# Performance work log

Measured on AMD Instinct MI355X. Metric: run time of the kernel, lower is better.

Reference implementation:

```python
import jax, jax.numpy as jnp
import numpy as np

N_NODES = 100000
N_EDGES = 3200000
N_GRAPHS = 2048
IN_FEATS = 64
HIDDEN = 128
EXTRA = 8


def setup_inputs() -> dict:
    key = jax.random.key(0)
    ks = jax.random.split(key, 16)
    inp = {
        "feats_node": jax.random.normal(ks[0], (N_NODES, IN_FEATS), jnp.float32),
        "feats_graph": jax.random.normal(ks[1], (N_GRAPHS, EXTRA), jnp.float32),
        "src": jax.random.randint(ks[2], (N_EDGES,), 0, N_NODES, jnp.int32),
        "dst": jax.random.randint(ks[3], (N_EDGES,), 0, N_NODES, jnp.int32),
        "graph_ids": jnp.sort(jax.random.randint(ks[4], (N_NODES,), 0, N_GRAPHS, jnp.int32)),
        # GCN weights (std=0.5 init, zero bias as in the torch module)
        "W1": jax.random.normal(ks[5], (IN_FEATS, HIDDEN), jnp.float32) * 0.5,
        "b1": jnp.zeros((HIDDEN,), jnp.float32),
        "W2": jax.random.normal(ks[6], (HIDDEN, HIDDEN), jnp.float32) * 0.5,
        "b2": jnp.zeros((HIDDEN,), jnp.float32),
        "W3": jax.random.normal(ks[7], (HIDDEN, HIDDEN), jnp.float32) * 0.5,
        "b3": jnp.zeros((HIDDEN,), jnp.float32),
        # MLP: (HIDDEN+EXTRA) -> 2*HIDDEN -> HIDDEN -> 1
        "M1": jax.random.normal(ks[8], (HIDDEN + EXTRA, 2 * HIDDEN), jnp.float32) * 0.5,
        "c1": jnp.zeros((2 * HIDDEN,), jnp.float32),
        "M2": jax.random.normal(ks[9], (2 * HIDDEN, HIDDEN), jnp.float32) * 0.5,
        "c2": jnp.zeros((HIDDEN,), jnp.float32),
        "M3": jax.random.normal(ks[10], (HIDDEN, 1), jnp.float32) * 0.5,
        "c3": jnp.zeros((1,), jnp.float32),
    }
    return inp


def _gcn_layer(h, W, b, src, dst, norm_src, norm_dst):
    # DGL GraphConv, norm='both': h' = D_in^{-1/2} A (D_out^{-1/2} h W) + b
    h = (h * norm_src[:, None]) @ W            # [N, out]
    agg = jax.ops.segment_sum(h[src], dst, num_segments=N_NODES)  # scatter-add over edges
    return agg * norm_dst[:, None] + b


def reference(feats_node, feats_graph, src, dst, graph_ids,
              W1, b1, W2, b2, W3, b3, M1, c1, M2, c2, M3, c3):
    ones_e = jnp.ones((N_EDGES,), jnp.float32)
    out_deg = jax.ops.segment_sum(ones_e, src, num_segments=N_NODES)
    in_deg = jax.ops.segment_sum(ones_e, dst, num_segments=N_NODES)
    norm_src = jax.lax.rsqrt(jnp.maximum(out_deg, 1.0))
    norm_dst = jax.lax.rsqrt(jnp.maximum(in_deg, 1.0))

    h = _gcn_layer(feats_node, W1, b1, src, dst, norm_src, norm_dst)
    h = jax.nn.selu(h)
    h = _gcn_layer(h, W2, b2, src, dst, norm_src, norm_dst)
    h = jax.nn.selu(h)
    h = _gcn_layer(h, W3, b3, src, dst, norm_src, norm_dst)
    h = jax.nn.selu(h)

    # AvgPooling readout: mean node features per graph
    sums = jax.ops.segment_sum(h, graph_ids, num_segments=N_GRAPHS)  # [G, H]
    cnts = jax.ops.segment_sum(jnp.ones((N_NODES,), jnp.float32), graph_ids, num_segments=N_GRAPHS)
    emb = sums / jnp.maximum(cnts, 1.0)[:, None]

    z = jnp.concatenate([emb, feats_graph], axis=1)  # [G, H+EXTRA]
    z = jax.nn.selu(z @ M1 + c1)
    z = jax.nn.selu(z @ M2 + c2)
    return z @ M3 + c3  # [G, 1]
```

## Files before the change

### kernel.cpp

```cpp
#include <hip/hip_runtime.h>
#include <hip/hip_bf16.h>
#include <cstddef>

#define N_NODES 100000
#define N_EDGES 3200000
#define N_GRAPHS 2048
#define IN_FEATS 64
#define HIDDEN 128
#define EXTRA 8

#define SCAN_CHUNK 1024
#define NB_CHUNKS ((N_NODES + SCAN_CHUNK - 1) / SCAN_CHUNK)

#define R_BINS 64000
#define NPASS 2
#define G_SORT 256
#define CHUNK (N_EDGES / G_SORT)

typedef unsigned short bf16_t;
typedef short bfx8 __attribute__((ext_vector_type(8)));
typedef float f32x4 __attribute__((ext_vector_type(4)));

__device__ __forceinline__ float selu_f(float x) {
    const float scale = 1.0507009873554805f;
    const float alpha = 1.6732632423543772f;
    return x > 0.f ? scale * x : scale * alpha * (__expf(x) - 1.f);
}
__device__ __forceinline__ float bf2f(unsigned short u) {
    union { unsigned int i; float f; } c; c.i = ((unsigned int)u) << 16; return c.f;
}
__device__ __forceinline__ unsigned short f2bf(float f) {
    union { float f; unsigned int i; } c; c.f = f;
    unsigned int lsb = (c.i >> 16) & 1;
    c.i += 0x7fffu + lsb;
    return (unsigned short)(c.i >> 16);
}


__global__ __launch_bounds__(512) void histo_kernel(const int* __restrict__ src,
                                                    const int* __restrict__ dst,
                                                    unsigned char* __restrict__ h_src,
                                                    unsigned char* __restrict__ h_dst) {
    __shared__ unsigned int hist[R_BINS / 4];
    const int b = blockIdx.x, t = threadIdx.x;
    const int e0 = b * CHUNK;
#pragma unroll
    for (int ph = 0; ph < 2; ++ph) {
        const int4* key4 = (const int4*)((ph ? src : dst) + e0);
        unsigned char* hout = (ph ? h_src : h_dst) + (size_t)b * N_NODES;
        for (int p = 0; p < NPASS; ++p) {
            const int r0 = p * R_BINS;
            const int rend = min(R_BINS, N_NODES - r0);
            for (int i = t; i < R_BINS / 4; i += 512) hist[i] = 0;
            __syncthreads();
            for (int i = t; i < CHUNK / 4; i += 512) {
                int4 k = key4[i];
                unsigned int x;
                x = (unsigned)(k.x - r0); if (x < (unsigned)R_BINS) atomicAdd(&hist[x >> 2], 1u << ((x & 3) << 3));
                x = (unsigned)(k.y - r0); if (x < (unsigned)R_BINS) atomicAdd(&hist[x >> 2], 1u << ((x & 3) << 3));
                x = (unsigned)(k.z - r0); if (x < (unsigned)R_BINS) atomicAdd(&hist[x >> 2], 1u << ((x & 3) << 3));
                x = (unsigned)(k.w - r0); if (x < (unsigned)R_BINS) atomicAdd(&hist[x >> 2], 1u << ((x & 3) << 3));
            }
            __syncthreads();
            unsigned int* ho4 = (unsigned int*)(hout + r0);
            for (int i = t; i < rend / 4; i += 512) ho4[i] = hist[i];
            __syncthreads();
        }
    }
}

__global__ __launch_bounds__(256) void degs_kernel(const unsigned char* __restrict__ h_src,
                                                   unsigned char* __restrict__ h_dst,
                                                   int* __restrict__ indeg,
                                                   float* __restrict__ nsrc,
                                                   float* __restrict__ ndst) {
    int bin = blockIdx.x * 256 + threadIdx.x;
    if (bin >= N_NODES) return;
    int s = 0;
#pragma unroll 8
    for (int b = 0; b < G_SORT; ++b) s += h_src[(size_t)b * N_NODES + bin];
    nsrc[bin] = rsqrtf(fmaxf((float)s, 1.f));
    int run = 0;
#pragma unroll 8
    for (int b = 0; b < G_SORT; ++b) {
        size_t off = (size_t)b * N_NODES + bin;
        int v = h_dst[off];
        h_dst[off] = (unsigned char)run;
        run += v;
    }
    indeg[bin] = run;
    ndst[bin] = rsqrtf(fmaxf((float)run, 1.f));
}

__global__ __launch_bounds__(512) void sortT_kernel(const int* __restrict__ src,
                                                    const int* __restrict__ dst,
                                                    const unsigned char* __restrict__ h_dst,
                                                    const int* __restrict__ rowptr,
                                                    int* __restrict__ csr_src) {
    __shared__ unsigned int cnt[R_BINS / 4];
    const int b = blockIdx.x, t = threadIdx.x;
    const int e0 = b * CHUNK;
    const int4* d4p = (const int4*)(dst + e0);
    const int4* s4p = (const int4*)(src + e0);
    const unsigned char* hrow = h_dst + (size_t)b * N_NODES;
    for (int p = 0; p < NPASS; ++p) {
        const int r0 = p * R_BINS;
        const int rend = min(R_BINS, N_NODES - r0);
        const unsigned int* hr4 = (const unsigned int*)(hrow + r0);
        for (int i = t; i < rend / 4; i += 512) cnt[i] = hr4[i];
        __syncthreads();
        for (int i = t; i < CHUNK / 4; i += 512) {
            int4 d = d4p[i];
            int4 s = s4p[i];
            unsigned int x, old, rank;
            x = (unsigned)(d.x - r0);
            if (x < (unsigned)R_BINS) {
                old = atomicAdd(&cnt[x >> 2], 1u << ((x & 3) << 3));
                rank = (old >> ((x & 3) << 3)) & 0xffu;
                csr_src[rowptr[d.x] + rank] = s.x;
            }
            x = (unsigned)(d.y - r0);
            if (x < (unsigned)R_BINS) {
                old = atomicAdd(&cnt[x >> 2], 1u << ((x & 3) << 3));
                rank = (old >> ((x & 3) << 3)) & 0xffu;
                csr_src[rowptr[d.y] + rank] = s.y;
            }
            x = (unsigned)(d.z - r0);
            if (x < (unsigned)R_BINS) {
                old = atomicAdd(&cnt[x >> 2], 1u << ((x & 3) << 3));
                rank = (old >> ((x & 3) << 3)) & 0xffu;
                csr_src[rowptr[d.z] + rank] = s.z;
            }
            x = (unsigned)(d.w - r0);
            if (x < (unsigned)R_BINS) {
                old = atomicAdd(&cnt[x >> 2], 1u << ((x & 3) << 3));
                rank = (old >> ((x & 3) << 3)) & 0xffu;
                csr_src[rowptr[d.w] + rank] = s.w;
            }
        }
        __syncthreads();
    }
}


__global__ __launch_bounds__(256) void scanA(const int* __restrict__ indeg,
                                             int* __restrict__ partials) {
    __shared__ int red[4];
    const int b = blockIdx.x, t = threadIdx.x;
    int base = b * SCAN_CHUNK + t * 4;
    int s = 0;
#pragma unroll
    for (int k = 0; k < 4; ++k) { int i = base + k; if (i < N_NODES) s += indeg[i]; }
    for (int off = 32; off; off >>= 1) s += __shfl_down(s, off);
    if ((t & 63) == 0) red[t >> 6] = s;
    __syncthreads();
    if (t == 0) partials[b] = red[0] + red[1] + red[2] + red[3];
}

__global__ __launch_bounds__(128) void scanB(int* __restrict__ partials,
                                             int* __restrict__ rowptr) {
    __shared__ int s[128];
    const int t = threadIdx.x;
    int v = (t < NB_CHUNKS) ? partials[t] : 0;
    s[t] = v;
    __syncthreads();
    for (int off = 1; off < 128; off <<= 1) {
        int u = (t >= off) ? s[t - off] : 0;
        __syncthreads();
        s[t] += u;
        __syncthreads();
    }
    if (t < NB_CHUNKS) partials[t] = s[t] - v;
    if (t == 127) rowptr[N_NODES] = s[127];
}

__global__ __launch_bounds__(256) void scanC(const int* __restrict__ indeg,
                                             const int* __restrict__ partials,
                                             int* __restrict__ rowptr) {
    __shared__ int ts[256];
    const int b = blockIdx.x, t = threadIdx.x;
    int base = b * SCAN_CHUNK + t * 4;
    int v[4];
    int s = 0;
#pragma unroll
    for (int k = 0; k < 4; ++k) { int i = base + k; v[k] = (i < N_NODES) ? indeg[i] : 0; s += v[k]; }
    ts[t] = s;
    __syncthreads();
    for (int off = 1; off < 256; off <<= 1) {
        int u = (t >= off) ? ts[t - off] : 0;
        __syncthreads();
        ts[t] += u;
        __syncthreads();
    }
    int excl = ts[t] - s + partials[b];
#pragma unroll
    for (int k = 0; k < 4; ++k) {
        int i = base + k;
        if (i < N_NODES) rowptr[i] = excl;
        excl += v[k];
    }
}

__global__ __launch_bounds__(256) void wprep_kernel(const float* __restrict__ W,
                                                    bf16_t* __restrict__ Wt, int K) {
    int i = blockIdx.x * 256 + threadIdx.x;
    if (i >= 128 * K) return;
    int n = i / K, k = i - n * K;
    Wt[i] = f2bf(W[k * 128 + n]);
}

__global__ __launch_bounds__(256) void prescale_kernel(const float* __restrict__ x,
                                                       const float* __restrict__ nsrc,
                                                       bf16_t* __restrict__ xb) {
    int i = blockIdx.x * 256 + threadIdx.x;
    const int total = N_NODES * (IN_FEATS / 4);
    if (i >= total) return;
    int node = i >> 4;
    float nm = nsrc[node];
    float4 v = ((const float4*)x)[i];
    ushort4 o;
    o.x = f2bf(v.x * nm); o.y = f2bf(v.y * nm);
    o.z = f2bf(v.z * nm); o.w = f2bf(v.w * nm);
    ((ushort4*)xb)[i] = o;
}

__global__ __launch_bounds__(256) void gather64_kernel(const bf16_t* __restrict__ xb,
                                                       const int* __restrict__ rowptr,
                                                       const int* __restrict__ csr_src,
                                                       const float* __restrict__ ndst,
                                                       bf16_t* __restrict__ outb) {
    const int l = threadIdx.x & 63;
    const int q = l >> 4;
    const int s16 = l & 15;
    const int node = (blockIdx.x * 256 + threadIdx.x) >> 6;
    if (node >= N_NODES) return;
    const int r0 = rowptr[node], r1 = rowptr[node + 1];
    float a0 = 0.f, a1 = 0.f, a2 = 0.f, a3 = 0.f;
    for (int base = r0; base < r1; base += 16) {
        const int nb = min(16, r1 - base);
        int myidx = __builtin_nontemporal_load(&csr_src[base + min(s16, nb - 1)]);
#pragma unroll
        for (int j = 0; j < 16; j += 4) {
            if (j >= nb) break;
            int e = j + q;
            int s = __shfl(myidx, min(e, nb - 1));
            if (e < nb) {
                ushort4 u = *(const ushort4*)(xb + (size_t)s * IN_FEATS + s16 * 4);
                a0 += bf2f(u.x); a1 += bf2f(u.y); a2 += bf2f(u.z); a3 += bf2f(u.w);
            }
        }
    }
    a0 += __shfl_xor(a0, 16); a1 += __shfl_xor(a1, 16);
    a2 += __shfl_xor(a2, 16); a3 += __shfl_xor(a3, 16);
    a0 += __shfl_xor(a0, 32); a1 += __shfl_xor(a1, 32);
    a2 += __shfl_xor(a2, 32); a3 += __shfl_xor(a3, 32);
    if (q == 0) {
        float nm = ndst[node];
        ushort4 o;
        o.x = f2bf(a0 * nm); o.y = f2bf(a1 * nm);
        o.z = f2bf(a2 * nm); o.w = f2bf(a3 * nm);
        *(ushort4*)(outb + (size_t)node * IN_FEATS + s16 * 4) = o;
    }
}

__global__ __launch_bounds__(256) void gather128_kernel(const bf16_t* __restrict__ hb,
                                                        const int* __restrict__ rowptr,
                                                        const int* __restrict__ csr_src,
                                                        const float* __restrict__ ndst,
                                                        bf16_t* __restrict__ outb) {
    const int l = threadIdx.x & 63;
    const int half = l >> 5;
    const int sub = l & 31;
    const int node = (blockIdx.x * 256 + threadIdx.x) >> 6;
    if (node >= N_NODES) return;
    const int r0 = rowptr[node], r1 = rowptr[node + 1];
    float a0 = 0.f, a1 = 0.f, a2 = 0.f, a3 = 0.f;
    for (int base = r0; base < r1; base += 32) {
        const int nb = min(32, r1 - base);
        int myidx = __builtin_nontemporal_load(&csr_src[base + min(sub, nb - 1)]);
#pragma unroll 8
        for (int j = 0; j < nb; j += 2) {
            int e = j + half;
            int s = __shfl(myidx, min(e, nb - 1));
            if (e < nb) {
                ushort4 u = *(const ushort4*)(hb + (size_t)s * HIDDEN + sub * 4);
                a0 += bf2f(u.x); a1 += bf2f(u.y); a2 += bf2f(u.z); a3 += bf2f(u.w);
            }
        }
    }
    a0 += __shfl_xor(a0, 32); a1 += __shfl_xor(a1, 32);
    a2 += __shfl_xor(a2, 32); a3 += __shfl_xor(a3, 32);
    if (half == 0) {
        float nm = ndst[node];
        ushort4 o;
        o.x = f2bf(a0 * nm); o.y = f2bf(a1 * nm);
        o.z = f2bf(a2 * nm); o.w = f2bf(a3 * nm);
        *(ushort4*)(outb + (size_t)node * HIDDEN + sub * 4) = o;
    }
}

template <int K, bool SCALE_OUT>
__global__ __launch_bounds__(256) void node_matmul_mfma(const bf16_t* __restrict__ Hb,
                                                        const bf16_t* __restrict__ Wt,
                                                        const float* __restrict__ bias,
                                                        const float* __restrict__ nsrc,
                                                        bf16_t* __restrict__ outb) {
    __shared__ char sW[128 * K * 2];
    const int t = threadIdx.x;

    for (int fb = t * 16; fb < 128 * K * 2; fb += 256 * 16) {
        bfx8 v = *(const bfx8*)((const char*)Wt + fb);
        int n = fb / (2 * K);
        *(bfx8*)(sW + (fb ^ ((n & 7) << 4))) = v;
    }
    __syncthreads();

    const int wv = t >> 6;
    const int l  = t & 63;
    const int m  = l & 15;
    const int kb = l >> 4;
    const int row0 = blockIdx.x * 64 + wv * 16;

    int arow = row0 + m;
    if (arow > N_NODES - 1) arow = N_NODES - 1;
    const char* aptr = (const char*)(Hb + (size_t)arow * K);

    f32x4 acc[8];
#pragma unroll
    for (int f = 0; f < 8; ++f) acc[f] = (f32x4){0.f, 0.f, 0.f, 0.f};

#pragma unroll
    for (int kc = 0; kc < K / 32; ++kc) {
        bfx8 a = *(const bfx8*)(aptr + kc * 64 + kb * 16);
#pragma unroll
        for (int f = 0; f < 8; ++f) {
            int n = f * 16 + m;
            int off = n * (2 * K) + kc * 64 + kb * 16;
            off ^= (n & 7) << 4;
            bfx8 b = *(const bfx8*)(sW + off);
            acc[f] = __builtin_amdgcn_mfma_f32_16x16x32_bf16(a, b, acc[f], 0, 0, 0);
        }
    }

    int nodes[4];
    float nm[4];
#pragma unroll
    for (int j = 0; j < 4; ++j) {
        nodes[j] = row0 + kb * 4 + j;
        nm[j] = 1.f;
        if (SCALE_OUT && nodes[j] < N_NODES) nm[j] = nsrc[nodes[j]];
    }
#pragma unroll
    for (int f = 0; f < 8; ++f) {
        int feat = f * 16 + m;
        float bb = bias[feat];
#pragma unroll
        for (int j = 0; j < 4; ++j) {
            if (nodes[j] < N_NODES) {
                float v = selu_f(acc[f][j] + bb) * nm[j];
                outb[(size_t)nodes[j] * HIDDEN + feat] = f2bf(v);
            }
        }
    }
}

__global__ __launch_bounds__(256) void pool_kernel(const bf16_t* __restrict__ h,
                                                   const int* __restrict__ gid,
                                                   float* __restrict__ emb,
                                                   float* __restrict__ cnt) {
    const int lane = threadIdx.x & 63;
    const int wid = (blockIdx.x * 256 + threadIdx.x) >> 6;
    const int n0 = wid * 64;
    if (n0 >= N_NODES) return;
    const int nend = (n0 + 64 < N_NODES) ? n0 + 64 : N_NODES;
    int cur = gid[n0];
    float ax = 0.f, ay = 0.f, run = 0.f;
    for (int n = n0; n < nend; ++n) {
        int g = gid[n];
        if (g != cur) {
            atomicAdd(&emb[(size_t)cur * HIDDEN + lane * 2], ax);
            atomicAdd(&emb[(size_t)cur * HIDDEN + lane * 2 + 1], ay);
            if (lane == 0) atomicAdd(&cnt[cur], run);
            cur = g; ax = 0.f; ay = 0.f; run = 0.f;
        }
        ushort2 u = *(const ushort2*)(h + (size_t)n * HIDDEN + lane * 2);
        ax += bf2f(u.x); ay += bf2f(u.y);
        run += 1.f;
    }
    atomicAdd(&emb[(size_t)cur * HIDDEN + lane * 2], ax);
    atomicAdd(&emb[(size_t)cur * HIDDEN + lane * 2 + 1], ay);
    if (lane == 0) atomicAdd(&cnt[cur], run);
}

__global__ __launch_bounds__(256) void mlp_kernel(const float* __restrict__ emb,
                                                  const float* __restrict__ cnt,
                                                  const float* __restrict__ fg,
                                                  const float* __restrict__ M1, const float* __restrict__ c1,
                                                  const float* __restrict__ M2, const float* __restrict__ c2,
                                                  const float* __restrict__ M3, const float* __restrict__ c3,
                                                  float* __restrict__ out) {
    const int g = blockIdx.x;
    const int t = threadIdx.x;
    __shared__ float z[HIDDEN + EXTRA];
    __shared__ float z1[2 * HIDDEN];
    __shared__ float z2[HIDDEN];
    if (t < HIDDEN) {
        float c = fmaxf(cnt[g], 1.f);
        z[t] = emb[(size_t)g * HIDDEN + t] / c;
    } else if (t < HIDDEN + EXTRA) {
        z[t] = fg[g * EXTRA + (t - HIDDEN)];
    }
    __syncthreads();
    {
        float s = c1[t];
        for (int k = 0; k < HIDDEN + EXTRA; ++k) s += z[k] * M1[k * (2 * HIDDEN) + t];
        z1[t] = selu_f(s);
    }
    __syncthreads();
    if (t < HIDDEN) {
        float s = c2[t];
        for (int k = 0; k < 2 * HIDDEN; ++k) s += z1[k] * M2[k * HIDDEN + t];
        z2[t] = selu_f(s);
    }
    __syncthreads();
    if (t < 64) {
        float s = z2[t] * M3[t] + z2[t + 64] * M3[t + 64];
#pragma unroll
        for (int off = 32; off; off >>= 1) s += __shfl_down(s, off);
        if (t == 0) out[g] = s + c3[0];
    }
}

extern "C" void kernel_launch(void* const* d_in, const int* in_sizes, int n_in,
                              void* d_out, int out_size, void* d_ws, size_t ws_size,
                              hipStream_t stream) {
    const float* feats_node  = (const float*)d_in[0];
    const float* feats_graph = (const float*)d_in[1];
    const int*   src         = (const int*)d_in[2];
    const int*   dst         = (const int*)d_in[3];
    const int*   gid         = (const int*)d_in[4];
    const float* W1 = (const float*)d_in[5];
    const float* b1 = (const float*)d_in[6];
    const float* W2 = (const float*)d_in[7];
    const float* b2 = (const float*)d_in[8];
    const float* W3 = (const float*)d_in[9];
    const float* b3 = (const float*)d_in[10];
    const float* M1 = (const float*)d_in[11];
    const float* c1 = (const float*)d_in[12];
    const float* M2 = (const float*)d_in[13];
    const float* c2 = (const float*)d_in[14];
    const float* M3 = (const float*)d_in[15];
    const float* c3 = (const float*)d_in[16];
    float* out = (float*)d_out;

    char* ws = (char*)d_ws;
    int* indeg   = (int*)ws;  ws += (size_t)N_NODES * sizeof(int);
    int* rowptr  = (int*)ws;  ws += (size_t)(N_NODES + 4) * sizeof(int);
    int* partials= (int*)ws;  ws += 128 * sizeof(int);
    float* norm_src = (float*)ws; ws += (size_t)N_NODES * sizeof(float);
    float* norm_dst = (float*)ws; ws += (size_t)N_NODES * sizeof(float);
    bf16_t* Wt1 = (bf16_t*)ws; ws += (size_t)128 * IN_FEATS * sizeof(bf16_t);
    bf16_t* Wt2 = (bf16_t*)ws; ws += (size_t)128 * HIDDEN * sizeof(bf16_t);
    bf16_t* Wt3 = (bf16_t*)ws; ws += (size_t)128 * HIDDEN * sizeof(bf16_t);
    int* csr_src = (int*)ws;  ws += (size_t)N_EDGES * sizeof(int);
    bf16_t* bufB = (bf16_t*)ws; ws += (size_t)N_NODES * HIDDEN * sizeof(bf16_t);
    unsigned char* h_dst = (unsigned char*)ws;
    bf16_t* bufA = (bf16_t*)ws;
    ws += (size_t)G_SORT * N_NODES;
    unsigned char* h_src = (unsigned char*)ws;
    bf16_t* xb   = (bf16_t*)ws;
    float* emb   = (float*)(ws + (size_t)N_NODES * IN_FEATS * sizeof(bf16_t));
    float* cnt   = emb + (size_t)N_GRAPHS * HIDDEN;
    ws += (size_t)G_SORT * N_NODES;

    histo_kernel<<<G_SORT, 512, 0, stream>>>(src, dst, h_src, h_dst);
    degs_kernel<<<(N_NODES + 255) / 256, 256, 0, stream>>>(h_src, h_dst, indeg, norm_src, norm_dst);
    scanA<<<NB_CHUNKS, 256, 0, stream>>>(indeg, partials);
    scanB<<<1, 128, 0, stream>>>(partials, rowptr);
    scanC<<<NB_CHUNKS, 256, 0, stream>>>(indeg, partials, rowptr);
    sortT_kernel<<<G_SORT, 512, 0, stream>>>(src, dst, h_dst, rowptr, csr_src);

    wprep_kernel<<<(128 * IN_FEATS + 255) / 256, 256, 0, stream>>>(W1, Wt1, IN_FEATS);
    wprep_kernel<<<(128 * HIDDEN + 255) / 256, 256, 0, stream>>>(W2, Wt2, HIDDEN);
    wprep_kernel<<<(128 * HIDDEN + 255) / 256, 256, 0, stream>>>(W3, Wt3, HIDDEN);
    prescale_kernel<<<(N_NODES * (IN_FEATS / 4) + 255) / 256, 256, 0, stream>>>(feats_node, norm_src, xb);

    const int mm_grid = (N_NODES + 63) / 64;
    const int g_grid  = (N_NODES + 3) / 4;

    gather64_kernel<<<g_grid, 256, 0, stream>>>(xb, rowptr, csr_src, norm_dst, bufA);
    node_matmul_mfma<IN_FEATS, true><<<mm_grid, 256, 0, stream>>>(bufA, Wt1, b1, norm_src, bufB);

    gather128_kernel<<<g_grid, 256, 0, stream>>>(bufB, rowptr, csr_src, norm_dst, bufA);
    node_matmul_mfma<HIDDEN, true><<<mm_grid, 256, 0, stream>>>(bufA, Wt2, b2, norm_src, bufB);

    gather128_kernel<<<g_grid, 256, 0, stream>>>(bufB, rowptr, csr_src, norm_dst, bufA);
    node_matmul_mfma<HIDDEN, false><<<mm_grid, 256, 0, stream>>>(bufA, Wt3, b3, norm_src, bufB);

    hipMemsetAsync(emb, 0, ((size_t)N_GRAPHS * HIDDEN + N_GRAPHS) * sizeof(float), stream);
    const int n_waves = (N_NODES + 63) / 64;
    pool_kernel<<<(n_waves + 3) / 4, 256, 0, stream>>>(bufB, gid, emb, cnt);
    mlp_kernel<<<N_GRAPHS, 256, 0, stream>>>(emb, cnt, feats_graph,
                                             M1, c1, M2, c2, M3, c3, out);
}
```

Before: 646.8 us.

## Fuse CSR neighbor gather into MFMA node matmul and merge weight prep launches

```diff
diff --git a/kernel.cpp b/kernel.cpp
--- a/kernel.cpp
+++ b/kernel.cpp
@@ -201,12 +201,29 @@
     }
 }
 
-__global__ __launch_bounds__(256) void wprep_kernel(const float* __restrict__ W,
-                                                    bf16_t* __restrict__ Wt, int K) {
+__global__ __launch_bounds__(256) void wprep_kernel(const float* __restrict__ W1,
+                                                    const float* __restrict__ W2,
+                                                    const float* __restrict__ W3,
+                                                    bf16_t* __restrict__ Wt1,
+                                                    bf16_t* __restrict__ Wt2,
+                                                    bf16_t* __restrict__ Wt3) {
     int i = blockIdx.x * 256 + threadIdx.x;
-    if (i >= 128 * K) return;
-    int n = i / K, k = i - n * K;
-    Wt[i] = f2bf(W[k * 128 + n]);
+    if (i < 128 * IN_FEATS) {
+        int n = i / IN_FEATS, k = i - n * IN_FEATS;
+        Wt1[i] = f2bf(W1[k * 128 + n]);
+        return;
+    }
+    i -= 128 * IN_FEATS;
+    if (i < 128 * HIDDEN) {
+        int n = i / HIDDEN, k = i - n * HIDDEN;
+        Wt2[i] = f2bf(W2[k * 128 + n]);
+        return;
+    }
+    i -= 128 * HIDDEN;
+    if (i < 128 * HIDDEN) {
+        int n = i / HIDDEN, k = i - n * HIDDEN;
+        Wt3[i] = f2bf(W3[k * 128 + n]);
+    }
 }
 
 __global__ __launch_bounds__(256) void prescale_kernel(const float* __restrict__ x,
@@ -224,88 +241,17 @@
     ((ushort4*)xb)[i] = o;
 }
 
-__global__ __launch_bounds__(256) void gather64_kernel(const bf16_t* __restrict__ xb,
-                                                       const int* __restrict__ rowptr,
-                                                       const int* __restrict__ csr_src,
-                                                       const float* __restrict__ ndst,
-                                                       bf16_t* __restrict__ outb) {
-    const int l = threadIdx.x & 63;
-    const int q = l >> 4;
-    const int s16 = l & 15;
-    const int node = (blockIdx.x * 256 + threadIdx.x) >> 6;
-    if (node >= N_NODES) return;
-    const int r0 = rowptr[node], r1 = rowptr[node + 1];
-    float a0 = 0.f, a1 = 0.f, a2 = 0.f, a3 = 0.f;
-    for (int base = r0; base < r1; base += 16) {
-        const int nb = min(16, r1 - base);
-        int myidx = __builtin_nontemporal_load(&csr_src[base + min(s16, nb - 1)]);
-#pragma unroll
-        for (int j = 0; j < 16; j += 4) {
-            if (j >= nb) break;
-            int e = j + q;
-            int s = __shfl(myidx, min(e, nb - 1));
-            if (e < nb) {
-                ushort4 u = *(const ushort4*)(xb + (size_t)s * IN_FEATS + s16 * 4);
-                a0 += bf2f(u.x); a1 += bf2f(u.y); a2 += bf2f(u.z); a3 += bf2f(u.w);
-            }
-        }
-    }
-    a0 += __shfl_xor(a0, 16); a1 += __shfl_xor(a1, 16);
-    a2 += __shfl_xor(a2, 16); a3 += __shfl_xor(a3, 16);
-    a0 += __shfl_xor(a0, 32); a1 += __shfl_xor(a1, 32);
-    a2 += __shfl_xor(a2, 32); a3 += __shfl_xor(a3, 32);
-    if (q == 0) {
-        float nm = ndst[node];
-        ushort4 o;
-        o.x = f2bf(a0 * nm); o.y = f2bf(a1 * nm);
-        o.z = f2bf(a2 * nm); o.w = f2bf(a3 * nm);
-        *(ushort4*)(outb + (size_t)node * IN_FEATS + s16 * 4) = o;
-    }
-}
-
-__global__ __launch_bounds__(256) void gather128_kernel(const bf16_t* __restrict__ hb,
-                                                        const int* __restrict__ rowptr,
-                                                        const int* __restrict__ csr_src,
-                                                        const float* __restrict__ ndst,
-                                                        bf16_t* __restrict__ outb) {
-    const int l = threadIdx.x & 63;
-    const int half = l >> 5;
-    const int sub = l & 31;
-    const int node = (blockIdx.x * 256 + threadIdx.x) >> 6;
-    if (node >= N_NODES) return;
-    const int r0 = rowptr[node], r1 = rowptr[node + 1];
-    float a0 = 0.f, a1 = 0.f, a2 = 0.f, a3 = 0.f;
-    for (int base = r0; base < r1; base += 32) {
-        const int nb = min(32, r1 - base);
-        int myidx = __builtin_nontemporal_load(&csr_src[base + min(sub, nb - 1)]);
-#pragma unroll 8
-        for (int j = 0; j < nb; j += 2) {
-            int e = j + half;
-            int s = __shfl(myidx, min(e, nb - 1));
-            if (e < nb) {
-                ushort4 u = *(const ushort4*)(hb + (size_t)s * HIDDEN + sub * 4);
-                a0 += bf2f(u.x); a1 += bf2f(u.y); a2 += bf2f(u.z); a3 += bf2f(u.w);
-            }
-        }
-    }
-    a0 += __shfl_xor(a0, 32); a1 += __shfl_xor(a1, 32);
-    a2 += __shfl_xor(a2, 32); a3 += __shfl_xor(a3, 32);
-    if (half == 0) {
-        float nm = ndst[node];
-        ushort4 o;
-        o.x = f2bf(a0 * nm); o.y = f2bf(a1 * nm);
-        o.z = f2bf(a2 * nm); o.w = f2bf(a3 * nm);
-        *(ushort4*)(outb + (size_t)node * HIDDEN + sub * 4) = o;
-    }
-}
-
 template <int K, bool SCALE_OUT>
-__global__ __launch_bounds__(256) void node_matmul_mfma(const bf16_t* __restrict__ Hb,
-                                                        const bf16_t* __restrict__ Wt,
-                                                        const float* __restrict__ bias,
-                                                        const float* __restrict__ nsrc,
-                                                        bf16_t* __restrict__ outb) {
+__global__ __launch_bounds__(256) void gmm_kernel(const bf16_t* __restrict__ Hin,
+                                                  const int* __restrict__ rowptr,
+                                                  const int* __restrict__ csr_src,
+                                                  const float* __restrict__ ndst,
+                                                  const bf16_t* __restrict__ Wt,
+                                                  const float* __restrict__ bias,
+                                                  const float* __restrict__ nsrc,
+                                                  bf16_t* __restrict__ outb) {
     __shared__ char sW[128 * K * 2];
+    __shared__ char sT[64 * K * 2];
     const int t = threadIdx.x;
 
     for (int fb = t * 16; fb < 128 * K * 2; fb += 256 * 16) {
@@ -317,13 +263,83 @@
 
     const int wv = t >> 6;
     const int l  = t & 63;
+    const int row0 = blockIdx.x * 64 + wv * 16;
+
+    if (K == 128) {
+        const int half = l >> 5;
+        const int sub  = l & 31;
+        for (int i = 0; i < 16; ++i) {
+            const int node = row0 + i;
+            float a0 = 0.f, a1 = 0.f, a2 = 0.f, a3 = 0.f;
+            if (node < N_NODES) {
+                const int r0 = rowptr[node], r1 = rowptr[node + 1];
+                for (int base = r0; base < r1; base += 32) {
+                    const int nb = min(32, r1 - base);
+                    int myidx = __builtin_nontemporal_load(&csr_src[base + min(sub, nb - 1)]);
+#pragma unroll 8
+                    for (int j = 0; j < nb; j += 2) {
+                        int e = j + half;
+                        int s = __shfl(myidx, min(e, nb - 1));
+                        if (e < nb) {
+                            ushort4 u = *(const ushort4*)(Hin + (size_t)s * K + sub * 4);
+                            a0 += bf2f(u.x); a1 += bf2f(u.y); a2 += bf2f(u.z); a3 += bf2f(u.w);
+                        }
+                    }
+                }
+            }
+            a0 += __shfl_xor(a0, 32); a1 += __shfl_xor(a1, 32);
+            a2 += __shfl_xor(a2, 32); a3 += __shfl_xor(a3, 32);
+            if (half == 0) {
+                float nm = (node < N_NODES) ? ndst[node] : 0.f;
+                ushort4 o;
+                o.x = f2bf(a0 * nm); o.y = f2bf(a1 * nm);
+                o.z = f2bf(a2 * nm); o.w = f2bf(a3 * nm);
+                int row = wv * 16 + i;
+                int off = row * (2 * K) + sub * 8;
+                *(ushort4*)(sT + (off ^ ((row & 7) << 4))) = o;
+            }
+        }
+    } else {
+        const int q   = l >> 4;
+        const int s16 = l & 15;
+        for (int i = 0; i < 16; ++i) {
+            const int node = row0 + i;
+            float a0 = 0.f, a1 = 0.f, a2 = 0.f, a3 = 0.f;
+            if (node < N_NODES) {
+                const int r0 = rowptr[node], r1 = rowptr[node + 1];
+                for (int base = r0; base < r1; base += 16) {
+                    const int nb = min(16, r1 - base);
+                    int myidx = __builtin_nontemporal_load(&csr_src[base + min(s16, nb - 1)]);
+#pragma unroll
+                    for (int j = 0; j < 16; j += 4) {
+                        if (j >= nb) break;
+                        int e = j + q;
+                        int s = __shfl(myidx, min(e, nb - 1));
+                        if (e < nb) {
+                            ushort4 u = *(const ushort4*)(Hin + (size_t)s * K + s16 * 4);
+                            a0 += bf2f(u.x); a1 += bf2f(u.y); a2 += bf2f(u.z); a3 += bf2f(u.w);
+                        }
+                    }
+                }
+            }
+            a0 += __shfl_xor(a0, 16); a1 += __shfl_xor(a1, 16);
+            a2 += __shfl_xor(a2, 16); a3 += __shfl_xor(a3, 16);
+            a0 += __shfl_xor(a0, 32); a1 += __shfl_xor(a1, 32);
+            a2 += __shfl_xor(a2, 32); a3 += __shfl_xor(a3, 32);
+            if (q == 0) {
+                float nm = (node < N_NODES) ? ndst[node] : 0.f;
+                ushort4 o;
+                o.x = f2bf(a0 * nm); o.y = f2bf(a1 * nm);
+                o.z = f2bf(a2 * nm); o.w = f2bf(a3 * nm);
+                int row = wv * 16 + i;
+                int off = row * (2 * K) + s16 * 8;
+                *(ushort4*)(sT + (off ^ ((row & 7) << 4))) = o;
+            }
+        }
+    }
+
     const int m  = l & 15;
     const int kb = l >> 4;
-    const int row0 = blockIdx.x * 64 + wv * 16;
-
-    int arow = row0 + m;
-    if (arow > N_NODES - 1) arow = N_NODES - 1;
-    const char* aptr = (const char*)(Hb + (size_t)arow * K);
 
     f32x4 acc[8];
 #pragma unroll
@@ -331,7 +347,10 @@
 
 #pragma unroll
     for (int kc = 0; kc < K / 32; ++kc) {
-        bfx8 a = *(const bfx8*)(aptr + kc * 64 + kb * 16);
+        int arow = wv * 16 + m;
+        int aoff = arow * (2 * K) + kc * 64 + kb * 16;
+        aoff ^= (arow & 7) << 4;
+        bfx8 a = *(const bfx8*)(sT + aoff);
 #pragma unroll
         for (int f = 0; f < 8; ++f) {
             int n = f * 16 + m;
@@ -480,22 +499,15 @@
     scanC<<<NB_CHUNKS, 256, 0, stream>>>(indeg, partials, rowptr);
     sortT_kernel<<<G_SORT, 512, 0, stream>>>(src, dst, h_dst, rowptr, csr_src);
 
-    wprep_kernel<<<(128 * IN_FEATS + 255) / 256, 256, 0, stream>>>(W1, Wt1, IN_FEATS);
-    wprep_kernel<<<(128 * HIDDEN + 255) / 256, 256, 0, stream>>>(W2, Wt2, HIDDEN);
-    wprep_kernel<<<(128 * HIDDEN + 255) / 256, 256, 0, stream>>>(W3, Wt3, HIDDEN);
+    const int wtot = 128 * IN_FEATS + 2 * 128 * HIDDEN;
+    wprep_kernel<<<(wtot + 255) / 256, 256, 0, stream>>>(W1, W2, W3, Wt1, Wt2, Wt3);
     prescale_kernel<<<(N_NODES * (IN_FEATS / 4) + 255) / 256, 256, 0, stream>>>(feats_node, norm_src, xb);
 
-    const int mm_grid = (N_NODES + 63) / 64;
-    const int g_grid  = (N_NODES + 3) / 4;
-
-    gather64_kernel<<<g_grid, 256, 0, stream>>>(xb, rowptr, csr_src, norm_dst, bufA);
-    node_matmul_mfma<IN_FEATS, true><<<mm_grid, 256, 0, stream>>>(bufA, Wt1, b1, norm_src, bufB);
-
-    gather128_kernel<<<g_grid, 256, 0, stream>>>(bufB, rowptr, csr_src, norm_dst, bufA);
-    node_matmul_mfma<HIDDEN, true><<<mm_grid, 256, 0, stream>>>(bufA, Wt2, b2, norm_src, bufB);
-
-    gather128_kernel<<<g_grid, 256, 0, stream>>>(bufB, rowptr, csr_src, norm_dst, bufA);
-    node_matmul_mfma<HIDDEN, false><<<mm_grid, 256, 0, stream>>>(bufA, Wt3, b3, norm_src, bufB);
+    const int gmm_grid = (N_NODES + 63) / 64;
+
+    gmm_kernel<IN_FEATS, true><<<gmm_grid, 256, 0, stream>>>(xb, rowptr, csr_src, norm_dst, Wt1, b1, norm_src, bufB);
+    gmm_kernel<HIDDEN, true><<<gmm_grid, 256, 0, stream>>>(bufB, rowptr, csr_src, norm_dst, Wt2, b2, norm_src, bufA);
+    gmm_kernel<HIDDEN, false><<<gmm_grid, 256, 0, stream>>>(bufA, rowptr, csr_src, norm_dst, Wt3, b3, norm_src, bufB);
 
     hipMemsetAsync(emb, 0, ((size_t)N_GRAPHS * HIDDEN + N_GRAPHS) * sizeof(float), stream);
     const int n_waves = (N_NODES + 63) / 64;
```

Result: slower. 1.177 ms (+82.0%).
